# Optimization experiments

Hardware: AMD Instinct MI355X
Metric: run time of the kernel (lower is better)

## Reference

```python
import jax, jax.numpy as jnp
import numpy as np

BN_EPS = 1e-3  # Keras BatchNormalization default epsilon


def _conv_block(x, k):
    """Per-task conv (stride 2, pad 1) -> ReLU -> BatchNorm (center/scale=False, training).

    x: [B, E, H, W, Cin]  (B tasks, E examples per task)
    k: [B, kh, kw, Cin, Cout]  per-task kernel
    """
    def conv_one(xe, kt):  # xe: [E,H,W,Cin], kt: [kh,kw,Cin,Cout]
        return jax.lax.conv_general_dilated(
            xe, kt, window_strides=(2, 2), padding=[(1, 1), (1, 1)],
            dimension_numbers=('NHWC', 'HWIO', 'NHWC'))
    y = jax.nn.relu(jax.vmap(conv_one)(x, k))  # [B,E,H',W',Cout]
    # BatchNorm in training mode: moments over all axes except channels
    m = jnp.mean(y, axis=(0, 1, 2, 3))
    v = jnp.var(y, axis=(0, 1, 2, 3))
    return (y - m) * jax.lax.rsqrt(v + BN_EPS)


def setup_inputs() -> dict:
    key = jax.random.key(0)
    ks = jax.random.split(key, 6)
    B, E, H, C, O = 64, 64, 28, 64, 20
    return {
        'x': jax.random.normal(ks[0], (B, E, H, H, 1), dtype=jnp.float32),
        'k1': jax.random.normal(ks[1], (B, 3, 3, 1, C), dtype=jnp.float32) * 0.1,
        'k2': jax.random.normal(ks[2], (B, 3, 3, C, C), dtype=jnp.float32) * 0.05,
        'k3': jax.random.normal(ks[3], (B, 3, 3, C, C), dtype=jnp.float32) * 0.05,
        'k4': jax.random.normal(ks[4], (B, 3, 3, C, C), dtype=jnp.float32) * 0.05,
        'w_ro': jax.random.normal(ks[5], (B, C, O), dtype=jnp.float32) * 0.1,
    }


def reference(x, k1, k2, k3, k4, w_ro):
    h = _conv_block(x, k1)   # [B,E,14,14,C]
    h = _conv_block(h, k2)   # [B,E,7,7,C]
    h = _conv_block(h, k3)   # [B,E,4,4,C]
    h = _conv_block(h, k4)   # [B,E,2,2,C]
    # MaxPooling2D with pool size == full spatial extent -> global spatial max
    feat = jnp.max(h, axis=(2, 3))  # [B,E,C]
    # per-task readout matmul: [B,E,H] x [B,H,O] -> [B,E,O]
    return jnp.einsum('beh,bho->beo', feat, w_ro)
```

## Files before the change

### kernel.cpp

```cpp
#include <hip/hip_runtime.h>

#define BN_EPS 1e-3f

typedef __attribute__((ext_vector_type(8))) short bf16x8;
typedef __attribute__((ext_vector_type(16))) float floatx16;
typedef unsigned short u16;

__device__ __forceinline__ u16 f2bf(float f) {
  unsigned u = __float_as_uint(f);
  u += 0x7fffu + ((u >> 16) & 1u);
  return (u16)(u >> 16);
}
__device__ __forceinline__ float bf2f(u16 h) {
  return __uint_as_float(((unsigned)h) << 16);
}

static constexpr int NSHARD = 64;

__global__ __launch_bounds__(256, 5) void conv1_k(
    const float* __restrict__ x, const float* __restrict__ k1,
    u16* __restrict__ y1, float* __restrict__ statsSh)
{
  __shared__ __align__(16) u16 smem1[13824];
  __shared__ __align__(16) float xp[30 * 36];
  __shared__ float redsum[64], redss[64];

  u16* Ah = smem1;
  u16* Al = smem1 + 5376;
  u16* Wh = smem1 + 10752;
  u16* Wl = smem1 + 12288;

  const int be = blockIdx.x, b = be >> 6, tid = threadIdx.x;

  {
    const uint4 z = uint4{0, 0, 0, 0};
    for (int i = tid; i < 1728; i += 256) ((uint4*)smem1)[i] = z;
    for (int i = tid; i < 270; i += 256) ((uint4*)xp)[i] = z;
    if (tid < 64) { redsum[tid] = 0.f; redss[tid] = 0.f; }
  }
  __syncthreads();

  for (int i = tid; i < 784; i += 256) {
    const int r = i / 28, c = i - 28 * r;
    xp[(r + 1) * 36 + (c + 1)] = x[(size_t)be * 784 + i];
  }
  for (int idx = tid; idx < 576; idx += 256) {
    const int t = idx >> 6, c = idx & 63;
    const float v = k1[(size_t)b * 576 + idx];
    const u16 hi = f2bf(v);
    const u16 lo = f2bf(v - bf2f(hi));
    Wh[c * 24 + t] = hi;
    Wl[c * 24 + t] = lo;
  }
  __syncthreads();

  if (tid < 196) {
    const int oy = tid / 14, ox = tid - 14 * oy;
    const float* base = &xp[(2 * oy) * 36 + 2 * ox];
#pragma unroll
    for (int ky = 0; ky < 3; ++ky)
#pragma unroll
      for (int kx = 0; kx < 3; ++kx) {
        const float v = base[ky * 36 + kx];
        const u16 hi = f2bf(v);
        const u16 lo = f2bf(v - bf2f(hi));
        Ah[tid * 24 + ky * 3 + kx] = hi;
        Al[tid * 24 + ky * 3 + kx] = lo;
      }
  }
  __syncthreads();

  const int wave = tid >> 6, lane = tid & 63;
  const int l31 = lane & 31, kq = (lane >> 5) * 8;

  bf16x8 ah[2], al[2], bh[2], bl[2];
#pragma unroll
  for (int mt = 0; mt < 2; ++mt) {
    const int row = (wave * 2 + mt) * 32 + l31;
    ah[mt] = *(const bf16x8*)&Ah[row * 24 + kq];
    al[mt] = *(const bf16x8*)&Al[row * 24 + kq];
  }
#pragma unroll
  for (int nt = 0; nt < 2; ++nt) {
    const int colB = nt * 32 + l31;
    bh[nt] = *(const bf16x8*)&Wh[colB * 24 + kq];
    bl[nt] = *(const bf16x8*)&Wl[colB * 24 + kq];
  }

  floatx16 acc[2][2];
#pragma unroll
  for (int mt = 0; mt < 2; ++mt)
#pragma unroll
    for (int nt = 0; nt < 2; ++nt) {
#pragma unroll
      for (int r = 0; r < 16; ++r) acc[mt][nt][r] = 0.f;
      acc[mt][nt] = __builtin_amdgcn_mfma_f32_32x32x16_bf16(
          al[mt], bh[nt], acc[mt][nt], 0, 0, 0);
      acc[mt][nt] = __builtin_amdgcn_mfma_f32_32x32x16_bf16(
          ah[mt], bl[nt], acc[mt][nt], 0, 0, 0);
      acc[mt][nt] = __builtin_amdgcn_mfma_f32_32x32x16_bf16(
          ah[mt], bh[nt], acc[mt][nt], 0, 0, 0);
    }

  __syncthreads();
  u16* yS = smem1;

#pragma unroll
  for (int nt = 0; nt < 2; ++nt) {
    const int col = nt * 32 + l31;
    float ls = 0.f, lss = 0.f;
#pragma unroll
    for (int mt = 0; mt < 2; ++mt) {
      const int rb = (wave * 2 + mt) * 32 + 4 * (lane >> 5);
#pragma unroll
      for (int r = 0; r < 16; ++r) {
        const int rw = rb + (r & 3) + 8 * (r >> 2);
        if (rw < 196) {
          const float v = fmaxf(acc[mt][nt][r], 0.f);
          yS[rw * 64 + col] = f2bf(v);
          ls += v;
          lss = fmaf(v, v, lss);
        }
      }
    }
    atomicAdd(&redsum[col], ls);
    atomicAdd(&redss[col], lss);
  }
  __syncthreads();

  {
    uint4* dst = (uint4*)(y1 + (size_t)be * 12544);
    const uint4* s4 = (const uint4*)yS;
    for (int i = tid; i < 1568; i += 256) dst[i] = s4[i];
  }
  if (tid < 64) {
    const int sh = be & (NSHARD - 1);
    atomicAdd(&statsSh[sh * 128 + tid], redsum[tid]);
    atomicAdd(&statsSh[sh * 128 + 64 + tid], redss[tid]);
  }
}

__global__ __launch_bounds__(256) void foldw_k(
    const float* __restrict__ W, const float* __restrict__ statsSh, float invN,
    u16* __restrict__ Wf, float* __restrict__ biasCls)
{
  __shared__ float T[64 * 68];
  __shared__ float P[256];
  __shared__ float s1[64], t1[64];
  __shared__ float tbS[64];

  const int b = blockIdx.x / 3, sg = blockIdx.x % 3;
  const int tid = threadIdx.x;

  {
    const int g = tid >> 7, cidx = tid & 127;
    float acc = 0.f;
    for (int k = 0; k < NSHARD / 2; ++k)
      acc += statsSh[(g * (NSHARD / 2) + k) * 128 + cidx];
    P[tid] = acc;
  }
  __syncthreads();
  if (tid < 64) {
    const float m = (P[tid] + P[tid + 128]) * invN;
    const float var = fmaf(-m, m, (P[64 + tid] + P[192 + tid]) * invN);
    const float s = rsqrtf(var + BN_EPS);
    s1[tid] = s;
    t1[tid] = -m * s;
  }
  __syncthreads();

  const int cin = tid >> 2, q0 = (tid & 3) * 16;
  const int cout = tid >> 2, ci0 = (tid & 3) * 16;
  for (int s = sg * 3; s < sg * 3 + 3; ++s) {
    if (tid < 64) tbS[tid] = 0.f;
    const float* ss = W + ((size_t)b * 9 + s) * 4096;
#pragma unroll
    for (int q = 0; q < 16; q += 4) {
      const float4 v = *(const float4*)(ss + cin * 64 + q0 + q);
      T[(q0 + q + 0) * 68 + cin] = v.x;
      T[(q0 + q + 1) * 68 + cin] = v.y;
      T[(q0 + q + 2) * 68 + cin] = v.z;
      T[(q0 + q + 3) * 68 + cin] = v.w;
    }
    __syncthreads();
    alignas(16) u16 tmp[16];
    float tb = 0.f;
#pragma unroll
    for (int j = 0; j < 16; ++j) {
      const float wv = T[cout * 68 + ci0 + j];
      tmp[j] = f2bf(wv * s1[ci0 + j]);
      tb = fmaf(t1[ci0 + j], wv, tb);
    }
    u16* dst = Wf + ((size_t)b * 9 + s) * 4096 + cout * 64 + ci0;
    *(uint4*)dst       = *(uint4*)&tmp[0];
    *(uint4*)(dst + 8) = *(uint4*)&tmp[8];
    atomicAdd(&tbS[cout], tb);
    __syncthreads();
    if (tid < 64) {
      const int ky = s / 3, kx = s % 3;
      const float tv = tbS[tid];
#pragma unroll
      for (int cls = 0; cls < 9; ++cls) {
        const int ry = cls / 3, rx = cls % 3;
        const bool valid = !((ry == 1 && ky == 0) || (ry == 2 && ky == 2) ||
                             (rx == 1 && kx == 0) || (rx == 2 && kx == 2));
        if (valid) atomicAdd(&biasCls[(size_t)b * 576 + cls * 64 + tid], tv);
      }
    }
    __syncthreads();
  }
}

template <int Hin, int Hout, int G>
__device__ __forceinline__ void conv_core(
    const u16* __restrict__ yin, const u16* __restrict__ Wf,
    const float* __restrict__ biasCls, u16* __restrict__ yout,
    float* __restrict__ statsSh, int blk)
{
  constexpr int PPI  = Hout * Hout;
  constexpr int ROWS = G * PPI;
  constexpr int BPT  = 64 / G;
  constexpr int MR   = G * Hin * Hin;
  constexpr int ZR   = MR;
  constexpr int MS   = MR + 1;

  __shared__ __align__(16) u16 mapS[MS * 72];
  __shared__ __align__(16) u16 B2[8 * 64 * 8];
  __shared__ float biasS[576];
  __shared__ float redsum[64], redss[64];

  const int b = blk / BPT, e0 = (blk % BPT) * G;
  const int tid = threadIdx.x, lane = tid & 63, wave = tid >> 6;

  for (int i = tid; i < 576; i += 256) biasS[i] = biasCls[(size_t)b * 576 + i];
  if (tid < 64) { redsum[tid] = 0.f; redss[tid] = 0.f; }
  if (tid < 8) *(uint4*)&mapS[ZR * 72 + tid * 8] = uint4{0, 0, 0, 0};

  {
    const u16* src = yin + (size_t)(b * 64 + e0) * (Hin * Hin) * 64;
    for (int ch = tid; ch < MR * 8; ch += 256) {
      const int r = ch >> 3, c8 = ch & 7;
      *(uint4*)&mapS[r * 72 + c8 * 8] = *(const uint4*)(src + ch * 8);
    }
  }

  const int bco = tid >> 2, bq0 = (tid & 3) * 16, c8a = bq0 >> 3;
  const u16* wb = Wf + (size_t)b * 9 * 4096 + bco * 64 + bq0;
  {
    uint4 b0 = *(const uint4*)wb;
    uint4 b1 = *(const uint4*)(wb + 8);
    *(uint4*)&B2[((c8a + 0) * 64 + bco) * 8] = b0;
    *(uint4*)&B2[((c8a + 1) * 64 + bco) * 8] = b1;
  }

  const int m0 = (wave & 1) * 32, n0 = (wave >> 1) * 32;
  const int l31 = lane & 31, kh = lane >> 5;
  const int lrow = m0 + l31;
  const bool rv = lrow < ROWS;
  const int img = rv ? lrow / PPI : 0;
  const int pp  = rv ? lrow % PPI : 0;
  const int oy = pp / Hout, ox = pp % Hout;
  const int bcol = n0 + l31;

  floatx16 acc;
#pragma unroll
  for (int r = 0; r < 16; ++r) acc[r] = 0.f;

  __syncthreads();

#pragma unroll
  for (int s = 0; s < 9; ++s) {
    uint4 nb0, nb1;
    if (s < 8) {
      const u16* wsl = wb + (s + 1) * 4096;
      nb0 = *(const uint4*)wsl;
      nb1 = *(const uint4*)(wsl + 8);
    }
    const int ky = s / 3, kx = s % 3;
    int pix = ZR;
    if (rv) {
      const int iy = 2 * oy - 1 + ky, ix = 2 * ox - 1 + kx;
      if ((unsigned)iy < (unsigned)Hin && (unsigned)ix < (unsigned)Hin)
        pix = img * (Hin * Hin) + iy * Hin + ix;
    }
    const u16* ap = &mapS[pix * 72 + kh * 8];
    bf16x8 a[4], bv[4];
#pragma unroll
    for (int kk = 0; kk < 4; ++kk) {
      a[kk]  = *(const bf16x8*)(ap + kk * 16);
      bv[kk] = *(const bf16x8*)&B2[((((kk << 1) | kh)) * 64 + bcol) * 8];
    }
#pragma unroll
    for (int kk = 0; kk < 4; ++kk)
      acc = __builtin_amdgcn_mfma_f32_32x32x16_bf16(a[kk], bv[kk], acc, 0, 0, 0);
    if (s < 8) {
      __syncthreads();
      *(uint4*)&B2[((c8a + 0) * 64 + bco) * 8] = nb0;
      *(uint4*)&B2[((c8a + 1) * 64 + bco) * 8] = nb1;
      __syncthreads();
    }
  }

  const int col = bcol;
  const int rb = m0 + 4 * (lane >> 5);
  float ls = 0.f, lss = 0.f;
#pragma unroll
  for (int r = 0; r < 16; ++r) {
    const int rw = rb + (r & 3) + 8 * (r >> 2);
    if (rw < ROWS) {
      const int re = rw / PPI, pr = rw % PPI;
      const int ooy = pr / Hout, oox = pr % Hout;
      const int ry = (ooy == 0) ? 1 : ((2 * ooy + 1 >= Hin) ? 2 : 0);
      const int rx = (oox == 0) ? 1 : ((2 * oox + 1 >= Hin) ? 2 : 0);
      const float v = fmaxf(acc[r] + biasS[(ry * 3 + rx) * 64 + col], 0.f);
      yout[((size_t)(b * 64 + e0 + re) * PPI + pr) * 64 + col] = f2bf(v);
      ls += v;
      lss = fmaf(v, v, lss);
    }
  }
  atomicAdd(&redsum[col], ls);
  atomicAdd(&redss[col], lss);
  __syncthreads();
  if (tid < 64) {
    const int sh = blk & (NSHARD - 1);
    atomicAdd(&statsSh[sh * 128 + tid], redsum[tid]);
    atomicAdd(&statsSh[sh * 128 + 64 + tid], redss[tid]);
  }
}

__global__ __launch_bounds__(256, 4) void cg2_k(
    const u16* __restrict__ yin, const u16* __restrict__ Wf,
    const float* __restrict__ biasCls, u16* __restrict__ yout,
    float* __restrict__ statsSh) {
  conv_core<14, 7, 1>(yin, Wf, biasCls, yout, statsSh, blockIdx.x);
}
__global__ __launch_bounds__(256, 4) void cg3_k(
    const u16* __restrict__ yin, const u16* __restrict__ Wf,
    const float* __restrict__ biasCls, u16* __restrict__ yout,
    float* __restrict__ statsSh) {
  conv_core<7, 4, 4>(yin, Wf, biasCls, yout, statsSh, blockIdx.x);
}
__global__ __launch_bounds__(256, 4) void cg4_k(
    const u16* __restrict__ yin, const u16* __restrict__ Wf,
    const float* __restrict__ biasCls, u16* __restrict__ yout,
    float* __restrict__ statsSh) {
  conv_core<4, 2, 16>(yin, Wf, biasCls, yout, statsSh, blockIdx.x);
}

__global__ __launch_bounds__(256) void readout_k(
    const u16* __restrict__ y4, const float* __restrict__ w_ro,
    const float* __restrict__ statsSh, float invN, float* __restrict__ outp)
{
  __shared__ float wl[64 * 20];
  __shared__ float feat[64 * 64];
  __shared__ float P[256];
  __shared__ float sArr[64], tArr[64];

  const int b = blockIdx.x, tid = threadIdx.x;

  {
    const int g = tid >> 7, cidx = tid & 127;
    float acc = 0.f;
    for (int k = 0; k < NSHARD / 2; ++k)
      acc += statsSh[(g * (NSHARD / 2) + k) * 128 + cidx];
    P[tid] = acc;
  }
  for (int i = tid; i < 1280; i += 256) wl[i] = w_ro[(size_t)b * 1280 + i];
  __syncthreads();
  if (tid < 64) {
    const float m = (P[tid] + P[tid + 128]) * invN;
    const float var = fmaf(-m, m, (P[64 + tid] + P[192 + tid]) * invN);
    const float s = rsqrtf(var + BN_EPS);
    sArr[tid] = s;
    tArr[tid] = -m * s;
  }
  __syncthreads();

  {
    const int e = tid & 63;
    for (int c = tid >> 6; c < 64; c += 4) {
      const u16* p4 = y4 + ((size_t)(b * 64 + e) * 4) * 64 + c;
      const float v = fmaxf(fmaxf(bf2f(p4[0]), bf2f(p4[64])),
                            fmaxf(bf2f(p4[128]), bf2f(p4[192])));
      feat[c * 64 + e] = fmaf(v, sArr[c], tArr[c]);
    }
  }
  __syncthreads();

  const int e = tid >> 2, og = (tid & 3) * 5;
  float acc[5] = {0.f, 0.f, 0.f, 0.f, 0.f};
  for (int c = 0; c < 64; ++c) {
    const float f = feat[c * 64 + e];
#pragma unroll
    for (int j = 0; j < 5; ++j) acc[j] = fmaf(f, wl[c * 20 + og + j], acc[j]);
  }
#pragma unroll
  for (int j = 0; j < 5; ++j)
    outp[((size_t)b * 64 + e) * 20 + og + j] = acc[j];
}

extern "C" void kernel_launch(void* const* d_in, const int* in_sizes, int n_in,
                              void* d_out, int out_size, void* d_ws, size_t ws_size,
                              hipStream_t stream) {
  (void)in_sizes; (void)n_in; (void)out_size; (void)ws_size;
  const float* x   = (const float*)d_in[0];
  const float* k1  = (const float*)d_in[1];
  const float* k2  = (const float*)d_in[2];
  const float* k3  = (const float*)d_in[3];
  const float* k4  = (const float*)d_in[4];
  const float* wro = (const float*)d_in[5];
  float* out = (float*)d_out;
  char* ws = (char*)d_ws;

  float* stats = (float*)ws;
  float* bias2 = (float*)(ws + 131072);
  float* bias3 = bias2 + 36864;
  float* bias4 = bias3 + 36864;
  u16* k2f = (u16*)(ws + 131072 + 442368);
  u16* k3f = k2f + (size_t)2359296;
  u16* k4f = k3f + (size_t)2359296;
  u16* y2 = k4f + (size_t)2359296;
  u16* y1 = y2 + (size_t)12845056;
  u16* y3 = y1;
  u16* y4 = y3 + (size_t)4194304;

  float* st1 = stats;
  float* st2 = stats + 8192;
  float* st3 = stats + 16384;
  float* st4 = stats + 24576;

  hipMemsetAsync(stats, 0, 131072 + 442368, stream);

  conv1_k<<<4096, 256, 0, stream>>>(x, k1, y1, st1);
  foldw_k<<<192, 256, 0, stream>>>(k2, st1, 1.f / 802816.f, k2f, bias2);
  cg2_k<<<4096, 256, 0, stream>>>(y1, k2f, bias2, y2, st2);
  foldw_k<<<192, 256, 0, stream>>>(k3, st2, 1.f / 200704.f, k3f, bias3);
  cg3_k<<<1024, 256, 0, stream>>>(y2, k3f, bias3, y3, st3);
  foldw_k<<<192, 256, 0, stream>>>(k4, st3, 1.f / 65536.f, k4f, bias4);
  cg4_k<<<256, 256, 0, stream>>>(y3, k4f, bias4, y4, st4);
  readout_k<<<64, 256, 0, stream>>>(y4, wro, st4, 1.f / 16384.f, out);
}
```

Before: 254.1 us.

## Fuse all conv/fold/readout stages into one persistent cooperative kernel with grid syncs

Replaces the eight separate kernel launches with a single cooperative persistent kernel whose blocks loop over the work items of each stage and meet at grid.sync barriers. All stages share one statically sized shared buffer. The goal is to remove per-launch overhead and the idle tails between stages. The trade-offs are seven grid-wide barriers, a grid capped at 1024 blocks, and an occupancy fixed by the largest shared footprint and register use of any stage. The last conv stage also changes from 16 to 8 images per block (512 blocks), which changes that stage's tiling.

Result: slower. 989.7 us (+289.4%).

```diff
diff --git a/kernel.cpp b/kernel.cpp
--- a/kernel.cpp
+++ b/kernel.cpp
@@ -1,6 +1,9 @@
 #include <hip/hip_runtime.h>
+#include <hip/hip_cooperative_groups.h>
 
 #define BN_EPS 1e-3f
+
+namespace cg = cooperative_groups;
 
 typedef __attribute__((ext_vector_type(8))) short bf16x8;
 typedef __attribute__((ext_vector_type(16))) float floatx16;
@@ -17,20 +20,21 @@
 
 static constexpr int NSHARD = 64;
 
-__global__ __launch_bounds__(256, 5) void conv1_k(
+__device__ __forceinline__ void conv1_body(
     const float* __restrict__ x, const float* __restrict__ k1,
-    u16* __restrict__ y1, float* __restrict__ statsSh)
+    u16* __restrict__ y1, float* __restrict__ statsSh, int be, char* SM)
 {
-  __shared__ __align__(16) u16 smem1[13824];
-  __shared__ __align__(16) float xp[30 * 36];
-  __shared__ float redsum[64], redss[64];
+  u16* smem1 = (u16*)SM;
+  float* xp = (float*)(SM + 27648);
+  float* redsum = (float*)(SM + 31968);
+  float* redss  = redsum + 64;
 
   u16* Ah = smem1;
   u16* Al = smem1 + 5376;
   u16* Wh = smem1 + 10752;
   u16* Wl = smem1 + 12288;
 
-  const int be = blockIdx.x, b = be >> 6, tid = threadIdx.x;
+  const int b = be >> 6, tid = threadIdx.x;
 
   {
     const uint4 z = uint4{0, 0, 0, 0};
@@ -138,18 +142,20 @@
     atomicAdd(&statsSh[sh * 128 + tid], redsum[tid]);
     atomicAdd(&statsSh[sh * 128 + 64 + tid], redss[tid]);
   }
-}
-
-__global__ __launch_bounds__(256) void foldw_k(
-    const float* __restrict__ W, const float* __restrict__ statsSh, float invN,
-    u16* __restrict__ Wf, float* __restrict__ biasCls)
+  __syncthreads();
+}
+
+__device__ __forceinline__ void foldw_body(
+    const float* __restrict__ W, const float* __restrict__ statsSh,
+    float invN, u16* __restrict__ Wf, float* __restrict__ biasCls,
+    int b, int sg, char* SM)
 {
-  __shared__ float T[64 * 68];
-  __shared__ float P[256];
-  __shared__ float s1[64], t1[64];
-  __shared__ float tbS[64];
-
-  const int b = blockIdx.x / 3, sg = blockIdx.x % 3;
+  float* T   = (float*)SM;
+  float* P   = (float*)(SM + 17408);
+  float* s1  = (float*)(SM + 18432);
+  float* t1  = (float*)(SM + 18688);
+  float* tbS = (float*)(SM + 18944);
+
   const int tid = threadIdx.x;
 
   {
@@ -212,10 +218,10 @@
 }
 
 template <int Hin, int Hout, int G>
-__device__ __forceinline__ void conv_core(
+__device__ __forceinline__ void conv_body(
     const u16* __restrict__ yin, const u16* __restrict__ Wf,
     const float* __restrict__ biasCls, u16* __restrict__ yout,
-    float* __restrict__ statsSh, int blk)
+    float* __restrict__ statsSh, int blk, char* SM)
 {
   constexpr int PPI  = Hout * Hout;
   constexpr int ROWS = G * PPI;
@@ -224,10 +230,11 @@
   constexpr int ZR   = MR;
   constexpr int MS   = MR + 1;
 
-  __shared__ __align__(16) u16 mapS[MS * 72];
-  __shared__ __align__(16) u16 B2[8 * 64 * 8];
-  __shared__ float biasS[576];
-  __shared__ float redsum[64], redss[64];
+  u16* mapS = (u16*)SM;
+  u16* B2   = (u16*)(SM + MS * 144);
+  float* biasS  = (float*)(SM + MS * 144 + 8192);
+  float* redsum = (float*)(SM + MS * 144 + 10496);
+  float* redss  = redsum + 64;
 
   const int b = blk / BPT, e0 = (blk % BPT) * G;
   const int tid = threadIdx.x, lane = tid & 63, wave = tid >> 6;
@@ -326,37 +333,21 @@
     atomicAdd(&statsSh[sh * 128 + tid], redsum[tid]);
     atomicAdd(&statsSh[sh * 128 + 64 + tid], redss[tid]);
   }
-}
-
-__global__ __launch_bounds__(256, 4) void cg2_k(
-    const u16* __restrict__ yin, const u16* __restrict__ Wf,
-    const float* __restrict__ biasCls, u16* __restrict__ yout,
-    float* __restrict__ statsSh) {
-  conv_core<14, 7, 1>(yin, Wf, biasCls, yout, statsSh, blockIdx.x);
-}
-__global__ __launch_bounds__(256, 4) void cg3_k(
-    const u16* __restrict__ yin, const u16* __restrict__ Wf,
-    const float* __restrict__ biasCls, u16* __restrict__ yout,
-    float* __restrict__ statsSh) {
-  conv_core<7, 4, 4>(yin, Wf, biasCls, yout, statsSh, blockIdx.x);
-}
-__global__ __launch_bounds__(256, 4) void cg4_k(
-    const u16* __restrict__ yin, const u16* __restrict__ Wf,
-    const float* __restrict__ biasCls, u16* __restrict__ yout,
-    float* __restrict__ statsSh) {
-  conv_core<4, 2, 16>(yin, Wf, biasCls, yout, statsSh, blockIdx.x);
-}
-
-__global__ __launch_bounds__(256) void readout_k(
+  __syncthreads();
+}
+
+__device__ __forceinline__ void readout_body(
     const u16* __restrict__ y4, const float* __restrict__ w_ro,
-    const float* __restrict__ statsSh, float invN, float* __restrict__ outp)
+    const float* __restrict__ statsSh, float invN, float* __restrict__ outp,
+    int b, char* SM)
 {
-  __shared__ float wl[64 * 20];
-  __shared__ float feat[64 * 64];
-  __shared__ float P[256];
-  __shared__ float sArr[64], tArr[64];
-
-  const int b = blockIdx.x, tid = threadIdx.x;
+  float* wl   = (float*)SM;
+  float* feat = (float*)(SM + 5120);
+  float* P    = (float*)(SM + 21504);
+  float* sArr = (float*)(SM + 22528);
+  float* tArr = (float*)(SM + 22784);
+
+  const int tid = threadIdx.x;
 
   {
     const int g = tid >> 7, cidx = tid & 127;
@@ -397,6 +388,57 @@
 #pragma unroll
   for (int j = 0; j < 5; ++j)
     outp[((size_t)b * 64 + e) * 20 + og + j] = acc[j];
+}
+
+__global__ __launch_bounds__(256, 4) void pipe_k(
+    const float* __restrict__ x,  const float* __restrict__ k1,
+    const float* __restrict__ k2, const float* __restrict__ k3,
+    const float* __restrict__ k4, const float* __restrict__ wro,
+    float* __restrict__ out, float* __restrict__ stats,
+    float* __restrict__ bias2, float* __restrict__ bias3,
+    float* __restrict__ bias4, u16* __restrict__ k2f,
+    u16* __restrict__ k3f, u16* __restrict__ k4f,
+    u16* __restrict__ y1, u16* __restrict__ y2,
+    u16* __restrict__ y3, u16* __restrict__ y4, int NG)
+{
+  __shared__ __align__(16) char SM[39424];
+  cg::grid_group grid = cg::this_grid();
+  const int bid = blockIdx.x;
+
+  float* st1 = stats;
+  float* st2 = stats + 8192;
+  float* st3 = stats + 16384;
+  float* st4 = stats + 24576;
+
+  for (int be = bid; be < 4096; be += NG) conv1_body(x, k1, y1, st1, be, SM);
+  __threadfence(); grid.sync();
+
+  for (int i = bid; i < 192; i += NG)
+    foldw_body(k2, st1, 1.f / 802816.f, k2f, bias2, i / 3, i % 3, SM);
+  __threadfence(); grid.sync();
+
+  for (int blk = bid; blk < 4096; blk += NG)
+    conv_body<14, 7, 1>(y1, k2f, bias2, y2, st2, blk, SM);
+  __threadfence(); grid.sync();
+
+  for (int i = bid; i < 192; i += NG)
+    foldw_body(k3, st2, 1.f / 200704.f, k3f, bias3, i / 3, i % 3, SM);
+  __threadfence(); grid.sync();
+
+  for (int blk = bid; blk < 1024; blk += NG)
+    conv_body<7, 4, 4>(y2, k3f, bias3, y3, st3, blk, SM);
+  __threadfence(); grid.sync();
+
+  for (int i = bid; i < 192; i += NG)
+    foldw_body(k4, st3, 1.f / 65536.f, k4f, bias4, i / 3, i % 3, SM);
+  __threadfence(); grid.sync();
+
+  for (int blk = bid; blk < 512; blk += NG)
+    conv_body<4, 2, 8>(y3, k4f, bias4, y4, st4, blk, SM);
+  __threadfence(); grid.sync();
+
+  for (int i = bid; i < 64; i += NG)
+    readout_body(y4, wro, st4, 1.f / 16384.f, out, i, SM);
 }
 
 extern "C" void kernel_launch(void* const* d_in, const int* in_sizes, int n_in,
@@ -424,19 +466,19 @@
   u16* y3 = y1;
   u16* y4 = y3 + (size_t)4194304;
 
-  float* st1 = stats;
-  float* st2 = stats + 8192;
-  float* st3 = stats + 16384;
-  float* st4 = stats + 24576;
-
   hipMemsetAsync(stats, 0, 131072 + 442368, stream);
 
-  conv1_k<<<4096, 256, 0, stream>>>(x, k1, y1, st1);
-  foldw_k<<<192, 256, 0, stream>>>(k2, st1, 1.f / 802816.f, k2f, bias2);
-  cg2_k<<<4096, 256, 0, stream>>>(y1, k2f, bias2, y2, st2);
-  foldw_k<<<192, 256, 0, stream>>>(k3, st2, 1.f / 200704.f, k3f, bias3);
-  cg3_k<<<1024, 256, 0, stream>>>(y2, k3f, bias3, y3, st3);
-  foldw_k<<<192, 256, 0, stream>>>(k4, st3, 1.f / 65536.f, k4f, bias4);
-  cg4_k<<<256, 256, 0, stream>>>(y3, k4f, bias4, y4, st4);
-  readout_k<<<64, 256, 0, stream>>>(y4, wro, st4, 1.f / 16384.f, out);
-}
+  int nb = 0;
+  if (hipOccupancyMaxActiveBlocksPerMultiprocessor(&nb, pipe_k, 256, 0)
+          != hipSuccess || nb < 1)
+    nb = 1;
+  int NG = nb * 256;
+  if (NG > 1024) NG = 1024;
+
+  void* args[] = {
+      (void*)&x, (void*)&k1, (void*)&k2, (void*)&k3, (void*)&k4, (void*)&wro,
+      (void*)&out, (void*)&stats, (void*)&bias2, (void*)&bias3, (void*)&bias4,
+      (void*)&k2f, (void*)&k3f, (void*)&k4f,
+      (void*)&y1, (void*)&y2, (void*)&y3, (void*)&y4, (void*)&NG};
+  hipLaunchCooperativeKernel(pipe_k, dim3(NG), dim3(256), args, 0, stream);
+}
```

## Specialize conv2 kernel to load activations directly from global without LDS staging

Applied to the files above, without the earlier changes.

Replaces the generic conv_core instantiation for layer 2 with a dedicated kernel. Each lane gathers its im2col A fragments straight from global memory per 3x3 tap, and only the per-tap weight slice is staged in LDS, with the next tap's weights prefetched into registers. This removes the full input-map staging in shared memory and raises the occupancy target to 6 blocks. In exchange it relies on cache hits for the strided global gathers and adds two barriers per tap.

After: 265.1 us. +4.3%, slower.

```diff
diff --git a/kernel.cpp b/kernel.cpp
--- a/kernel.cpp
+++ b/kernel.cpp
@@ -208,6 +208,113 @@
       }
     }
     __syncthreads();
+  }
+}
+
+__global__ __launch_bounds__(256, 6) void cg2_k(
+    const u16* __restrict__ yin, const u16* __restrict__ Wf,
+    const float* __restrict__ biasCls, u16* __restrict__ yout,
+    float* __restrict__ statsSh)
+{
+  constexpr int Hin = 14, Hout = 7, PPI = 49, ROWS = 49;
+
+  __shared__ __align__(16) u16 B2[8 * 64 * 8];
+  __shared__ float biasS[576];
+  __shared__ float redsum[64], redss[64];
+
+  const int be = blockIdx.x, b = be >> 6;
+  const int tid = threadIdx.x, lane = tid & 63, wave = tid >> 6;
+
+  for (int i = tid; i < 576; i += 256) biasS[i] = biasCls[(size_t)b * 576 + i];
+  if (tid < 64) { redsum[tid] = 0.f; redss[tid] = 0.f; }
+
+  const int bco = tid >> 2, bq0 = (tid & 3) * 16, c8a = bq0 >> 3;
+  const u16* wb = Wf + (size_t)b * 9 * 4096 + bco * 64 + bq0;
+  {
+    uint4 b0 = *(const uint4*)wb;
+    uint4 b1 = *(const uint4*)(wb + 8);
+    *(uint4*)&B2[((c8a + 0) * 64 + bco) * 8] = b0;
+    *(uint4*)&B2[((c8a + 1) * 64 + bco) * 8] = b1;
+  }
+
+  const int m0 = (wave & 1) * 32, n0 = (wave >> 1) * 32;
+  const int l31 = lane & 31, kh = lane >> 5;
+  const int lrow = m0 + l31;
+  const bool rv = lrow < ROWS;
+  const int oy = rv ? lrow / Hout : 0, ox = rv ? lrow % Hout : 0;
+  const int bcol = n0 + l31;
+
+  const u16* ya = yin + (size_t)be * 12544 + kh * 8;
+
+  bf16x8 zz;
+#pragma unroll
+  for (int j = 0; j < 8; ++j) zz[j] = 0;
+
+  floatx16 acc;
+#pragma unroll
+  for (int r = 0; r < 16; ++r) acc[r] = 0.f;
+
+  __syncthreads();
+
+#pragma unroll
+  for (int s = 0; s < 9; ++s) {
+    uint4 nb0, nb1;
+    if (s < 8) {
+      const u16* wsl = wb + (s + 1) * 4096;
+      nb0 = *(const uint4*)wsl;
+      nb1 = *(const uint4*)(wsl + 8);
+    }
+    const int ky = s / 3, kx = s % 3;
+    const int iy = 2 * oy - 1 + ky, ix = 2 * ox - 1 + kx;
+    const bool va = rv && (unsigned)iy < (unsigned)Hin &&
+                    (unsigned)ix < (unsigned)Hin;
+    const u16* ap = ya + (iy * Hin + ix) * 64;
+
+    bf16x8 a[4], bv[4];
+    if (va) {
+#pragma unroll
+      for (int kk = 0; kk < 4; ++kk) a[kk] = *(const bf16x8*)(ap + kk * 16);
+    } else {
+#pragma unroll
+      for (int kk = 0; kk < 4; ++kk) a[kk] = zz;
+    }
+#pragma unroll
+    for (int kk = 0; kk < 4; ++kk)
+      bv[kk] = *(const bf16x8*)&B2[((((kk << 1) | kh)) * 64 + bcol) * 8];
+#pragma unroll
+    for (int kk = 0; kk < 4; ++kk)
+      acc = __builtin_amdgcn_mfma_f32_32x32x16_bf16(a[kk], bv[kk], acc, 0, 0, 0);
+    if (s < 8) {
+      __syncthreads();
+      *(uint4*)&B2[((c8a + 0) * 64 + bco) * 8] = nb0;
+      *(uint4*)&B2[((c8a + 1) * 64 + bco) * 8] = nb1;
+      __syncthreads();
+    }
+  }
+
+  const int col = bcol;
+  const int rb = m0 + 4 * (lane >> 5);
+  float ls = 0.f, lss = 0.f;
+#pragma unroll
+  for (int r = 0; r < 16; ++r) {
+    const int rw = rb + (r & 3) + 8 * (r >> 2);
+    if (rw < ROWS) {
+      const int ooy = rw / Hout, oox = rw % Hout;
+      const int ry = (ooy == 0) ? 1 : ((2 * ooy + 1 >= Hin) ? 2 : 0);
+      const int rx = (oox == 0) ? 1 : ((2 * oox + 1 >= Hin) ? 2 : 0);
+      const float v = fmaxf(acc[r] + biasS[(ry * 3 + rx) * 64 + col], 0.f);
+      yout[((size_t)be * PPI + rw) * 64 + col] = f2bf(v);
+      ls += v;
+      lss = fmaf(v, v, lss);
+    }
+  }
+  atomicAdd(&redsum[col], ls);
+  atomicAdd(&redss[col], lss);
+  __syncthreads();
+  if (tid < 64) {
+    const int sh = be & (NSHARD - 1);
+    atomicAdd(&statsSh[sh * 128 + tid], redsum[tid]);
+    atomicAdd(&statsSh[sh * 128 + 64 + tid], redss[tid]);
   }
 }
 
@@ -328,12 +435,6 @@
   }
 }
 
-__global__ __launch_bounds__(256, 4) void cg2_k(
-    const u16* __restrict__ yin, const u16* __restrict__ Wf,
-    const float* __restrict__ biasCls, u16* __restrict__ yout,
-    float* __restrict__ statsSh) {
-  conv_core<14, 7, 1>(yin, Wf, biasCls, yout, statsSh, blockIdx.x);
-}
 __global__ __launch_bounds__(256, 4) void cg3_k(
     const u16* __restrict__ yin, const u16* __restrict__ Wf,
     const float* __restrict__ biasCls, u16* __restrict__ yout,
```
